# Kernel optimization log

Hardware: AMD Instinct MI355X
Metric: run time of the kernel (lower is better)

Reference implementation:

```python
import jax, jax.numpy as jnp
import numpy as np

B, S, H = 2, 2048, 2048
NH, NKV, HD = 16, 4, 128
GROUPS = NH // NKV  # 4
ROPE_BASE = 10000.0


def _rope_tables(seq_len, dim):
    inv_freq = 1.0 / (ROPE_BASE ** (jnp.arange(0, dim, 2, dtype=jnp.float32) / dim))
    t = jnp.arange(seq_len, dtype=jnp.float32)
    freqs = jnp.outer(t, inv_freq)            # [S, HD/2]
    emb = jnp.concatenate([freqs, freqs], -1)  # [S, HD]
    return jnp.cos(emb), jnp.sin(emb)


def _rotate_half(x):
    x1, x2 = x[..., : x.shape[-1] // 2], x[..., x.shape[-1] // 2:]
    return jnp.concatenate([-x2, x1], axis=-1)


def setup_inputs() -> dict:
    key = jax.random.key(0)
    ks = jax.random.split(key, 5)
    hidden_states = jax.random.normal(ks[0], (B, S, H), dtype=jnp.float32)
    wq = jax.random.normal(ks[1], (H, NH * HD), dtype=jnp.float32) * 0.02
    wk = jax.random.normal(ks[2], (H, NKV * HD), dtype=jnp.float32) * 0.02
    wv = jax.random.normal(ks[3], (H, NKV * HD), dtype=jnp.float32) * 0.02
    wo = jax.random.normal(ks[4], (NH * HD, H), dtype=jnp.float32) * 0.02
    # additive causal mask [1,1,S,S]
    causal = jnp.tril(jnp.ones((S, S), dtype=bool))
    attention_mask = jnp.where(causal, 0.0, jnp.finfo(jnp.float32).min)[None, None]
    return {"hidden_states": hidden_states, "attention_mask": attention_mask,
            "wq": wq, "wk": wk, "wv": wv, "wo": wo}


def reference(hidden_states, attention_mask, wq, wk, wv, wo):
    b, s, _ = hidden_states.shape
    # projections -> [B, heads, S, HD]
    q = (hidden_states @ wq).reshape(b, s, NH, HD).transpose(0, 2, 1, 3)
    k = (hidden_states @ wk).reshape(b, s, NKV, HD).transpose(0, 2, 1, 3)
    v = (hidden_states @ wv).reshape(b, s, NKV, HD).transpose(0, 2, 1, 3)
    cos, sin = _rope_tables(s, HD)             # [S, HD]
    cos = cos[None, None]; sin = sin[None, None]
    q = q * cos + _rotate_half(q) * sin
    k = k * cos + _rotate_half(k) * sin
    # GQA: repeat kv heads (matches repeat_interleave on dim=1)
    k = jnp.repeat(k, GROUPS, axis=1)
    v = jnp.repeat(v, GROUPS, axis=1)
    scores = jnp.einsum("bhqd,bhkd->bhqk", q, k) / jnp.sqrt(jnp.float32(HD))
    scores = scores + attention_mask
    probs = jax.nn.softmax(scores.astype(jnp.float32), axis=-1).astype(q.dtype)
    attn = jnp.einsum("bhqk,bhkd->bhqd", probs, v)
    attn = attn.transpose(0, 2, 1, 3).reshape(b, s, NH * HD)
    return attn @ wo
```

## Files before the change

### kernel.cpp

```cpp
#include <hip/hip_runtime.h>

typedef unsigned short u16;
typedef unsigned int u32;
typedef __attribute__((ext_vector_type(8))) __bf16 bf16x8;
typedef __attribute__((ext_vector_type(8))) u16 u16x8;
typedef __attribute__((ext_vector_type(4))) float f32x4;

#define B_ 2
#define S_ 2048
#define H_ 2048
#define NH_ 16
#define NKV_ 4
#define HD_ 128
#define L2E 1.4426950408889634f

__device__ __forceinline__ u16 f2bf(float f) {
  u32 u = __builtin_bit_cast(u32, f);
  u32 r = (u + 0x7fffu + ((u >> 16) & 1u)) >> 16;
  return (u16)r;
}
__device__ __forceinline__ float bf2f(u16 v) {
  return __builtin_bit_cast(float, (u32)v << 16);
}
__device__ __forceinline__ void gl2lds16(const void* g, void* l) {
  __builtin_amdgcn_global_load_lds((const __attribute__((address_space(1))) u32*)g,
                                   (__attribute__((address_space(3))) u32*)l, 16, 0, 0);
}
__device__ __forceinline__ f32x4 mfma16(bf16x8 a, bf16x8 b, f32x4 c) {
  return __builtin_amdgcn_mfma_f32_16x16x32_bf16(a, b, c, 0, 0, 0);
}

__global__ __launch_bounds__(256) void cvt_f32_bf16(const float* __restrict__ in,
                                                    u16* __restrict__ out) {
  size_t i = ((size_t)blockIdx.x * 256 + threadIdx.x) * 8;
  const float4* p = (const float4*)(in + i);
  float4 a = p[0], b = p[1];
  u16x8 o;
  o[0] = f2bf(a.x); o[1] = f2bf(a.y); o[2] = f2bf(a.z); o[3] = f2bf(a.w);
  o[4] = f2bf(b.x); o[5] = f2bf(b.y); o[6] = f2bf(b.z); o[7] = f2bf(b.w);
  *(u16x8*)(out + i) = o;
}

__global__ __launch_bounds__(256) void transpose_f32_bf16(const float* __restrict__ in,
                                                          u16* __restrict__ out,
                                                          int R, int C) {
  __shared__ float tl[32][33];
  int bx = blockIdx.x, by = blockIdx.y;
  int tx = threadIdx.x & 31, ty = threadIdx.x >> 5;
#pragma unroll
  for (int i = 0; i < 32; i += 8)
    tl[ty + i][tx] = in[(size_t)(by * 32 + ty + i) * C + bx * 32 + tx];
  __syncthreads();
#pragma unroll
  for (int i = 0; i < 32; i += 8)
    out[(size_t)(bx * 32 + ty + i) * R + by * 32 + tx] = f2bf(tl[tx][ty + i]);
}

__global__ __launch_bounds__(256) void transpose_v(const u16* __restrict__ kvb,
                                                   u16* __restrict__ vt) {
  __shared__ u16 tl[32][33];
  int sx = blockIdx.x, dx = blockIdx.y, b = blockIdx.z;
  int tx = threadIdx.x & 31, ty = threadIdx.x >> 5;
#pragma unroll
  for (int i = 0; i < 32; i += 8)
    tl[ty + i][tx] = kvb[(size_t)(b * S_ + sx * 32 + ty + i) * 1024 + 512 + dx * 32 + tx];
  __syncthreads();
#pragma unroll
  for (int i = 0; i < 32; i += 8)
    vt[(size_t)(b * 512 + dx * 32 + ty + i) * 2048 + sx * 32 + tx] = tl[tx][ty + i];
}

__global__ __launch_bounds__(256) void rope_kernel(u16* __restrict__ buf, int rstride,
                                                   int nhshift, float scale) {
  int idx = blockIdx.x * 256 + threadIdx.x;
  int grp = idx & 7;
  int h = (idx >> 3) & ((1 << nhshift) - 1);
  int tok = idx >> (3 + nhshift);
  int s = tok & (S_ - 1);
  u16* p = buf + (size_t)tok * rstride + (h << 7) + grp * 8;
  u16x8 lo = *(u16x8*)p;
  u16x8 hi = *(u16x8*)(p + 64);
  u16x8 olo, ohi;
#pragma unroll
  for (int j = 0; j < 8; j++) {
    int i = grp * 8 + j;
    float inv = exp2f((float)i * -0.20762050593045702f);
    float ang = (float)s * inv;
    float c = cosf(ang) * scale, sn = sinf(ang) * scale;
    float xl = bf2f(lo[j]), xh = bf2f(hi[j]);
    olo[j] = f2bf(xl * c - xh * sn);
    ohi[j] = f2bf(xh * c + xl * sn);
  }
  *(u16x8*)p = olo;
  *(u16x8*)(p + 64) = ohi;
}

template <int MODE>
__global__ __launch_bounds__(256) void gemm_bt(const u16* __restrict__ A,
                                               const u16* __restrict__ BT,
                                               void* __restrict__ C0,
                                               void* __restrict__ C1,
                                               int M, int N, int K) {
  __shared__ u16 As[2 * 128 * 32];
  __shared__ u16 Bs[2 * 128 * 32];
  const int Mt = M >> 7;
  const int nwg = gridDim.x;
  int wg = (blockIdx.x & 7) * (nwg >> 3) + (blockIdx.x >> 3);
  int tm = wg % Mt, tn = wg / Mt;
  const size_t m0 = (size_t)tm << 7, n0 = (size_t)tn << 7;
  const int tid = threadIdx.x;
  const int w = tid >> 6, lane = tid & 63;
  const int g = lane >> 4, l15 = lane & 15;
  const int wr = w >> 1, wc = w & 1;

  const int r0 = tid >> 2, s0 = tid & 3;
  const int r1 = (tid + 256) >> 2, s1 = (tid + 256) & 3;
  const u16* Ar0 = A + (m0 + r0) * K + s0 * 8;
  const u16* Ar1 = A + (m0 + r1) * K + s1 * 8;
  const u16* Br0 = BT + (n0 + r0) * K + s0 * 8;
  const u16* Br1 = BT + (n0 + r1) * K + s1 * 8;

  const f32x4 Z4 = {0.f, 0.f, 0.f, 0.f};
  f32x4 acc[4][4];
#pragma unroll
  for (int m = 0; m < 4; m++)
#pragma unroll
    for (int n = 0; n < 4; n++) acc[m][n] = Z4;

  gl2lds16(Ar0, &As[w * 512]);
  gl2lds16(Ar1, &As[w * 512 + 2048]);
  gl2lds16(Br0, &Bs[w * 512]);
  gl2lds16(Br1, &Bs[w * 512 + 2048]);
  __syncthreads();

  const int nk = K >> 5;
  int cur = 0;
  for (int t = 0; t < nk; ++t) {
    if (t + 1 < nk) {
      const int k0 = (t + 1) << 5;
      const int nb = (cur ^ 1) << 12;
      gl2lds16(Ar0 + k0, &As[nb + w * 512]);
      gl2lds16(Ar1 + k0, &As[nb + w * 512 + 2048]);
      gl2lds16(Br0 + k0, &Bs[nb + w * 512]);
      gl2lds16(Br1 + k0, &Bs[nb + w * 512 + 2048]);
    }
    const int cb = cur << 12;
    bf16x8 af[4], bfr[4];
#pragma unroll
    for (int m = 0; m < 4; m++)
      af[m] = *(const bf16x8*)&As[cb + (wr * 64 + m * 16 + l15) * 32 + g * 8];
#pragma unroll
    for (int n = 0; n < 4; n++)
      bfr[n] = *(const bf16x8*)&Bs[cb + (wc * 64 + n * 16 + l15) * 32 + g * 8];
#pragma unroll
    for (int m = 0; m < 4; m++)
#pragma unroll
      for (int n = 0; n < 4; n++) acc[m][n] = mfma16(af[m], bfr[n], acc[m][n]);
    __syncthreads();
    cur ^= 1;
  }

  if (MODE == 2) {
    float* C = (float*)C0;
#pragma unroll
    for (int m = 0; m < 4; m++)
#pragma unroll
      for (int n = 0; n < 4; n++)
#pragma unroll
        for (int r = 0; r < 4; r++) {
          size_t row = m0 + wr * 64 + m * 16 + g * 4 + r;
          size_t col = n0 + wc * 64 + n * 16 + l15;
          C[row * (size_t)N + col] = acc[m][n][r];
        }
  } else {
    u16* C;
    size_t cs, cbase;
    if (n0 < 2048) { C = (u16*)C0; cs = 2048; cbase = n0; }
    else           { C = (u16*)C1; cs = 1024; cbase = n0 - 2048; }
#pragma unroll
    for (int m = 0; m < 4; m++)
#pragma unroll
      for (int n = 0; n < 4; n++)
#pragma unroll
        for (int r = 0; r < 4; r++) {
          size_t row = m0 + wr * 64 + m * 16 + g * 4 + r;
          C[row * cs + cbase + wc * 64 + n * 16 + l15] = f2bf(acc[m][n][r]);
        }
  }
}

__global__ __launch_bounds__(256) void attn_kernel(const u16* __restrict__ Qb,
                                                   const u16* __restrict__ KVb,
                                                   const u16* __restrict__ Vt,
                                                   u16* __restrict__ Ob) {
  __shared__ u16 Ks[64 * 128];
  __shared__ u16 Vs[128 * 64];
  __shared__ u16 Ps[4][16 * 72];
  const int pair = blockIdx.x, h = blockIdx.y, b = blockIdx.z;
  const int kvh = h >> 2;
  const int tid = threadIdx.x, w = tid >> 6, lane = tid & 63;
  const int g = lane >> 4, l15 = lane & 15;
  const f32x4 Z4 = {0.f, 0.f, 0.f, 0.f};

  for (int half = 0; half < 2; ++half) {
    const int qt = half ? pair : 31 - pair;
    const int qrow0 = qt * 64 + w * 16;

    bf16x8 qf[4];
    const u16* qp = Qb + (size_t)(b * S_ + qrow0 + l15) * 2048 + h * 128;
#pragma unroll
    for (int ds = 0; ds < 4; ds++) qf[ds] = *(const bf16x8*)(qp + ds * 32 + g * 8);

    float m_r[4], l_r[4];
    f32x4 oa[8];
#pragma unroll
    for (int r = 0; r < 4; r++) { m_r[r] = -1e30f; l_r[r] = 0.f; }
#pragma unroll
    for (int n = 0; n < 8; n++) oa[n] = Z4;

    const int nt = qt + 1;
    for (int t = 0; t < nt; ++t) {
      const int kv0 = t * 64;
#pragma unroll
      for (int ro = 0; ro < 4; ++ro) {
        int c = ro * 256 + tid;
        int kv = c >> 4, p = c & 15;
        gl2lds16(KVb + (size_t)(b * S_ + kv0 + kv) * 1024 + kvh * 128 + 8 * (p ^ (kv & 15)),
                 &Ks[ro * 2048 + w * 512]);
        int d = c >> 3, p2 = c & 7;
        gl2lds16(Vt + (size_t)((b * NKV_ + kvh) * HD_ + d) * 2048 + kv0 + 8 * (p2 ^ (d & 7)),
                 &Vs[ro * 2048 + w * 512]);
      }
      __syncthreads();

      f32x4 sa[4];
#pragma unroll
      for (int c16 = 0; c16 < 4; c16++) sa[c16] = Z4;
      __builtin_amdgcn_s_setprio(1);
#pragma unroll
      for (int ds = 0; ds < 4; ++ds) {
#pragma unroll
        for (int c16 = 0; c16 < 4; ++c16) {
          bf16x8 kf = *(const bf16x8*)&Ks[(c16 * 16 + l15) * 128 + ((ds * 4 + g) ^ l15) * 8];
          sa[c16] = mfma16(qf[ds], kf, sa[c16]);
        }
      }
      __builtin_amdgcn_s_setprio(0);

      if (kv0 + 63 > qrow0) {
#pragma unroll
        for (int c16 = 0; c16 < 4; c16++)
#pragma unroll
          for (int r = 0; r < 4; r++) {
            if (kv0 + c16 * 16 + l15 > qrow0 + g * 4 + r) sa[c16][r] = -1e30f;
          }
      }

      float pm[4];
#pragma unroll
      for (int r = 0; r < 4; r++)
        pm[r] = fmaxf(fmaxf(sa[0][r], sa[1][r]), fmaxf(sa[2][r], sa[3][r]));
#pragma unroll
      for (int off = 1; off < 16; off <<= 1)
#pragma unroll
        for (int r = 0; r < 4; r++) pm[r] = fmaxf(pm[r], __shfl_xor(pm[r], off));

      bool need = (pm[0] > m_r[0] + 8.f) || (pm[1] > m_r[1] + 8.f) ||
                  (pm[2] > m_r[2] + 8.f) || (pm[3] > m_r[3] + 8.f);
      if (__any(need)) {
#pragma unroll
        for (int r = 0; r < 4; r++) {
          float mn = fmaxf(m_r[r], pm[r]);
          float corr = exp2f((m_r[r] - mn) * L2E);
          m_r[r] = mn;
          l_r[r] *= corr;
#pragma unroll
          for (int n = 0; n < 8; n++) oa[n][r] *= corr;
        }
      }

      float p[4][4], rs[4];
#pragma unroll
      for (int r = 0; r < 4; r++) rs[r] = 0.f;
#pragma unroll
      for (int c16 = 0; c16 < 4; c16++)
#pragma unroll
        for (int r = 0; r < 4; r++) {
          p[c16][r] = exp2f((sa[c16][r] - m_r[r]) * L2E);
          rs[r] += p[c16][r];
        }
#pragma unroll
      for (int off = 1; off < 16; off <<= 1)
#pragma unroll
        for (int r = 0; r < 4; r++) rs[r] += __shfl_xor(rs[r], off);
#pragma unroll
      for (int r = 0; r < 4; r++) l_r[r] += rs[r];

#pragma unroll
      for (int c16 = 0; c16 < 4; c16++)
#pragma unroll
        for (int r = 0; r < 4; r++)
          Ps[w][(g * 4 + r) * 72 + c16 * 16 + l15] = f2bf(p[c16][r]);
      asm volatile("s_waitcnt lgkmcnt(0)" ::: "memory");
      __builtin_amdgcn_sched_barrier(0);

      __builtin_amdgcn_s_setprio(1);
#pragma unroll
      for (int ks = 0; ks < 2; ++ks) {
        bf16x8 pa = *(const bf16x8*)&Ps[w][l15 * 72 + ks * 32 + g * 8];
#pragma unroll
        for (int n = 0; n < 8; n++) {
          bf16x8 vf = *(const bf16x8*)&Vs[(n * 16 + l15) * 64 + (((ks * 4 + g) ^ (l15 & 7))) * 8];
          oa[n] = mfma16(pa, vf, oa[n]);
        }
      }
      __builtin_amdgcn_s_setprio(0);
      __syncthreads();
    }

    float inv[4];
#pragma unroll
    for (int r = 0; r < 4; r++) inv[r] = 1.0f / l_r[r];
#pragma unroll
    for (int n = 0; n < 8; n++)
#pragma unroll
      for (int r = 0; r < 4; r++) {
        size_t row = (size_t)b * S_ + qrow0 + g * 4 + r;
        Ob[row * 2048 + h * 128 + n * 16 + l15] = f2bf(oa[n][r] * inv[r]);
      }
  }
}

extern "C" void kernel_launch(void* const* d_in, const int* in_sizes, int n_in,
                              void* d_out, int out_size, void* d_ws, size_t ws_size,
                              hipStream_t stream) {
  const float* hid = (const float*)d_in[0];
  const float* wq = (const float*)d_in[2];
  const float* wk = (const float*)d_in[3];
  const float* wv = (const float*)d_in[4];
  const float* wo = (const float*)d_in[5];
  float* out = (float*)d_out;
  char* ws = (char*)d_ws;

  u16* hb     = (u16*)(ws);
  u16* wqkvT  = (u16*)(ws + (16u << 20));
  u16* Vt     = (u16*)(ws + (16u << 20));
  u16* woT    = (u16*)(ws + (20u << 20));
  u16* Qb     = (u16*)(ws + (28u << 20));
  u16* KVb    = (u16*)(ws + (44u << 20));

  cvt_f32_bf16<<<4096, 256, 0, stream>>>(hid, hb);
  transpose_f32_bf16<<<dim3(64, 64), 256, 0, stream>>>(wq, wqkvT, 2048, 2048);
  transpose_f32_bf16<<<dim3(16, 64), 256, 0, stream>>>(wk, wqkvT + (size_t)2048 * 2048, 2048, 512);
  transpose_f32_bf16<<<dim3(16, 64), 256, 0, stream>>>(wv, wqkvT + (size_t)2560 * 2048, 2048, 512);

  gemm_bt<1><<<768, 256, 0, stream>>>(hb, wqkvT, Qb, KVb, 4096, 3072, 2048);

  rope_kernel<<<2048, 256, 0, stream>>>(Qb, 2048, 4, 0.08838834764831845f);
  rope_kernel<<<512, 256, 0, stream>>>(KVb, 1024, 2, 1.0f);

  transpose_v<<<dim3(64, 16, 2), 256, 0, stream>>>(KVb, Vt);
  transpose_f32_bf16<<<dim3(64, 64), 256, 0, stream>>>(wo, woT, 2048, 2048);

  attn_kernel<<<dim3(16, 16, 2), 256, 0, stream>>>(Qb, KVb, Vt, hb);

  gemm_bt<2><<<512, 256, 0, stream>>>(hb, woT, out, nullptr, 4096, 2048, 2048);
}
```

Baseline: 254.9 us.

## Double-buffer K/V tiles in attention and compute row sums via MFMA

The attention kernel now keeps two LDS buffers for K and V and issues the loads for the next KV tile before computing on the current one, aiming to overlap global-to-LDS transfers with MFMA work. It also drops the shuffle-based reduction of softmax row sums and computes them with an extra MFMA of the bf16 probabilities against a vector of ones. This doubles K/V LDS usage, which may lower occupancy, and the row sum is now taken from bf16-rounded probabilities. It relies on the single barrier per iteration to order reuse of each buffer.

```diff
diff --git a/kernel.cpp b/kernel.cpp
--- a/kernel.cpp
+++ b/kernel.cpp
@@ -193,14 +193,21 @@
                                                    const u16* __restrict__ KVb,
                                                    const u16* __restrict__ Vt,
                                                    u16* __restrict__ Ob) {
-  __shared__ u16 Ks[64 * 128];
-  __shared__ u16 Vs[128 * 64];
+  __shared__ u16 Ks[2][64 * 128];
+  __shared__ u16 Vs[2][128 * 64];
   __shared__ u16 Ps[4][16 * 72];
   const int pair = blockIdx.x, h = blockIdx.y, b = blockIdx.z;
   const int kvh = h >> 2;
   const int tid = threadIdx.x, w = tid >> 6, lane = tid & 63;
   const int g = lane >> 4, l15 = lane & 15;
   const f32x4 Z4 = {0.f, 0.f, 0.f, 0.f};
+  u16x8 oneu;
+#pragma unroll
+  for (int j = 0; j < 8; j++) oneu[j] = 0x3f80;
+  const bf16x8 ones = __builtin_bit_cast(bf16x8, oneu);
+
+  const u16* Kbase = KVb + (size_t)b * S_ * 1024 + kvh * 128;
+  const u16* Vbase = Vt + (size_t)(b * NKV_ + kvh) * HD_ * 2048;
 
   for (int half = 0; half < 2; ++half) {
     const int qt = half ? pair : 31 - pair;
@@ -219,19 +226,32 @@
     for (int n = 0; n < 8; n++) oa[n] = Z4;
 
     const int nt = qt + 1;
+#pragma unroll
+    for (int ro = 0; ro < 4; ++ro) {
+      int c = ro * 256 + tid;
+      int kv = c >> 4, p = c & 15;
+      gl2lds16(Kbase + (size_t)kv * 1024 + 8 * (p ^ (kv & 15)), &Ks[0][ro * 2048 + w * 512]);
+      int d = c >> 3, p2 = c & 7;
+      gl2lds16(Vbase + (size_t)d * 2048 + 8 * (p2 ^ (d & 7)), &Vs[0][ro * 2048 + w * 512]);
+    }
+    __syncthreads();
+    int cur = 0;
+
     for (int t = 0; t < nt; ++t) {
       const int kv0 = t * 64;
-#pragma unroll
-      for (int ro = 0; ro < 4; ++ro) {
-        int c = ro * 256 + tid;
-        int kv = c >> 4, p = c & 15;
-        gl2lds16(KVb + (size_t)(b * S_ + kv0 + kv) * 1024 + kvh * 128 + 8 * (p ^ (kv & 15)),
-                 &Ks[ro * 2048 + w * 512]);
-        int d = c >> 3, p2 = c & 7;
-        gl2lds16(Vt + (size_t)((b * NKV_ + kvh) * HD_ + d) * 2048 + kv0 + 8 * (p2 ^ (d & 7)),
-                 &Vs[ro * 2048 + w * 512]);
-      }
-      __syncthreads();
+      if (t + 1 < nt) {
+        const int nkv0 = kv0 + 64;
+#pragma unroll
+        for (int ro = 0; ro < 4; ++ro) {
+          int c = ro * 256 + tid;
+          int kv = c >> 4, p = c & 15;
+          gl2lds16(Kbase + (size_t)(nkv0 + kv) * 1024 + 8 * (p ^ (kv & 15)),
+                   &Ks[cur ^ 1][ro * 2048 + w * 512]);
+          int d = c >> 3, p2 = c & 7;
+          gl2lds16(Vbase + (size_t)d * 2048 + nkv0 + 8 * (p2 ^ (d & 7)),
+                   &Vs[cur ^ 1][ro * 2048 + w * 512]);
+        }
+      }
 
       f32x4 sa[4];
 #pragma unroll
@@ -241,7 +261,7 @@
       for (int ds = 0; ds < 4; ++ds) {
 #pragma unroll
         for (int c16 = 0; c16 < 4; ++c16) {
-          bf16x8 kf = *(const bf16x8*)&Ks[(c16 * 16 + l15) * 128 + ((ds * 4 + g) ^ l15) * 8];
+          bf16x8 kf = *(const bf16x8*)&Ks[cur][(c16 * 16 + l15) * 128 + ((ds * 4 + g) ^ l15) * 8];
           sa[c16] = mfma16(qf[ds], kf, sa[c16]);
         }
       }
@@ -279,43 +299,33 @@
         }
       }
 
-      float p[4][4], rs[4];
-#pragma unroll
-      for (int r = 0; r < 4; r++) rs[r] = 0.f;
 #pragma unroll
       for (int c16 = 0; c16 < 4; c16++)
 #pragma unroll
-        for (int r = 0; r < 4; r++) {
-          p[c16][r] = exp2f((sa[c16][r] - m_r[r]) * L2E);
-          rs[r] += p[c16][r];
-        }
-#pragma unroll
-      for (int off = 1; off < 16; off <<= 1)
-#pragma unroll
-        for (int r = 0; r < 4; r++) rs[r] += __shfl_xor(rs[r], off);
-#pragma unroll
-      for (int r = 0; r < 4; r++) l_r[r] += rs[r];
-
-#pragma unroll
-      for (int c16 = 0; c16 < 4; c16++)
-#pragma unroll
         for (int r = 0; r < 4; r++)
-          Ps[w][(g * 4 + r) * 72 + c16 * 16 + l15] = f2bf(p[c16][r]);
+          Ps[w][(g * 4 + r) * 72 + c16 * 16 + l15] =
+              f2bf(exp2f((sa[c16][r] - m_r[r]) * L2E));
       asm volatile("s_waitcnt lgkmcnt(0)" ::: "memory");
       __builtin_amdgcn_sched_barrier(0);
 
+      f32x4 srow = Z4;
       __builtin_amdgcn_s_setprio(1);
 #pragma unroll
       for (int ks = 0; ks < 2; ++ks) {
         bf16x8 pa = *(const bf16x8*)&Ps[w][l15 * 72 + ks * 32 + g * 8];
+        srow = mfma16(pa, ones, srow);
 #pragma unroll
         for (int n = 0; n < 8; n++) {
-          bf16x8 vf = *(const bf16x8*)&Vs[(n * 16 + l15) * 64 + (((ks * 4 + g) ^ (l15 & 7))) * 8];
+          bf16x8 vf = *(const bf16x8*)&Vs[cur][(n * 16 + l15) * 64 + (((ks * 4 + g) ^ (l15 & 7))) * 8];
           oa[n] = mfma16(pa, vf, oa[n]);
         }
       }
       __builtin_amdgcn_s_setprio(0);
+#pragma unroll
+      for (int r = 0; r < 4; r++) l_r[r] += srow[r];
+
       __syncthreads();
+      cur ^= 1;
     }
 
     float inv[4];
```

Measured after the change: 247.5 us. 2.9% less time.
